# Performance work log

Hardware: AMD Instinct MI355X
Metric: run time of the kernel (lower is better)

## Reference

```python
import jax, jax.numpy as jnp
import numpy as np

N, D = 1024, 128
NEG_INF = -1e30


def setup_inputs() -> dict:
    key = jax.random.key(0)
    ks = jax.random.split(key, 8)
    s = 0.05
    return {
        "X": jax.random.normal(ks[0], (N, D), dtype=jnp.float32),
        "Wq": jax.random.normal(ks[1], (D, D), dtype=jnp.float32) * s,
        "Wk": jax.random.normal(ks[2], (D, D), dtype=jnp.float32) * s,
        "v": jax.random.normal(ks[3], (D,), dtype=jnp.float32) * s,
        "w_ih": jax.random.normal(ks[4], (3 * D, 2 * D), dtype=jnp.float32) * s,
        "w_hh": jax.random.normal(ks[5], (3 * D, D), dtype=jnp.float32) * s,
        "b_ih": jax.random.normal(ks[6], (3 * D,), dtype=jnp.float32) * s,
        "b_hh": jax.random.normal(ks[7], (3 * D,), dtype=jnp.float32) * s,
    }


def reference(X, Wq, Wk, v, w_ih, w_hh, b_ih, b_hh):
    n, d = X.shape
    # --- anti-causal additive attention (query i attends keys j >= i) ---
    q = X @ Wq.T                                   # (N, d)
    k = X @ Wk.T                                   # (N, d)
    # scores[i, j] = v . tanh(q_i + k_j)
    scores = jnp.einsum("ijd,d->ij", jnp.tanh(q[:, None, :] + k[None, :, :]), v)
    mask = jnp.arange(n)[None, :] >= jnp.arange(n)[:, None]   # suffix j >= i
    scores = jnp.where(mask, scores, NEG_INF)
    w = jax.nn.softmax(scores, axis=1)             # (N, N)
    att = w @ X                                    # (N, d) context over keys

    # --- single-layer GRU over the N "time" steps, batch 1 ---
    gru_in = jnp.concatenate((X, att), axis=1)     # (N, 2d)
    gi = gru_in @ w_ih.T + b_ih                    # (N, 3d) input gates, precomputed

    def step(h, gi_t):
        gh = h @ w_hh.T + b_hh                     # (3d,)
        i_r, i_z, i_n = jnp.split(gi_t, 3)
        h_r, h_z, h_n = jnp.split(gh, 3)
        r = jax.nn.sigmoid(i_r + h_r)
        z = jax.nn.sigmoid(i_z + h_z)
        nst = jnp.tanh(i_n + r * h_n)
        h_new = (1.0 - z) * nst + z * h
        return h_new, h_new

    h0 = jnp.zeros((d,), dtype=X.dtype)
    _, out = jax.lax.scan(step, h0, gi)            # (N, d)
    return out
```

## Files before the change

kernel.cpp:

```cpp
#include <hip/hip_runtime.h>
#include <hip/hip_bf16.h>

#define N 1024
#define D 128
#define SB 32
#define NSB (N / SB)

typedef __hip_bfloat16 bf16;
typedef __attribute__((ext_vector_type(8))) short bfx8;
typedef __attribute__((ext_vector_type(4))) float fx4;
typedef __attribute__((ext_vector_type(8))) unsigned short u16x8;

__device__ __forceinline__ float b2f(bf16 x) { return __bfloat162float(x); }
__device__ __forceinline__ short f2bf_bits(float x) {
    bf16 b = __float2bfloat16(x);
    return *reinterpret_cast<short*>(&b);
}
__device__ __forceinline__ float bfbits2f(unsigned short u) {
    return __uint_as_float(((unsigned int)u) << 16);
}
__device__ __forceinline__ float fastrcp(float x) { return __builtin_amdgcn_rcpf(x); }

__device__ __forceinline__ float fast_tanh(float x) {
    float e = __expf(2.f * x);
    return 1.f - 2.f * fastrcp(e + 1.f);
}
__device__ __forceinline__ float fast_sigmoid(float x) {
    return fastrcp(1.f + __expf(-x));
}

__device__ __forceinline__ float sel4(fx4 v, int r) {
    float x = (r & 1) ? v[1] : v[0];
    float y = (r & 1) ? v[3] : v[2];
    return (r & 2) ? y : x;
}

__device__ __forceinline__ void async_copy16(const float* g, void* l) {
    __builtin_amdgcn_global_load_lds((const __attribute__((address_space(1))) void*)g,
                                     (__attribute__((address_space(3))) void*)l, 16, 0, 0);
}

__global__ void sniff_kernel(const unsigned short* __restrict__ xu, int* __restrict__ flag) {
    int l = threadIdx.x;
    int cnt = 0;
#pragma unroll
    for (int k = 0; k < 8; ++k) {
        unsigned short u = xu[2 * (l * 8 + k)];
        int e = (u >> 7) & 0xFF;
        cnt += (e >= 96 && e <= 144) ? 1 : 0;
    }
    for (int off = 32; off > 0; off >>= 1) cnt += __shfl_down(cnt, off);
    if (l == 0) *flag = (cnt > 400) ? 1 : 0;
}

struct ConvArgs {
    const void* p[8];
    float* o[8];
    int n[8];
};
__global__ void convert_kernel(ConvArgs A, const int* __restrict__ flag) {
    int seg = blockIdx.y;
    int n = A.n[seg];
    int isbf = *flag;
    const void* p = A.p[seg];
    float* o = A.o[seg];
    for (int i = blockIdx.x * blockDim.x + threadIdx.x; i < n; i += gridDim.x * blockDim.x) {
        float v = isbf ? b2f(((const bf16*)p)[i]) : ((const float*)p)[i];
        o[i] = v;
    }
}

__global__ void transpose_wih(const float* __restrict__ wih, float* __restrict__ wihT) {
    int id = blockIdx.x * 256 + threadIdx.x;
    int c = id / 384;
    int o = id - c * 384;
    wihT[id] = wih[o * 256 + c];
}

__global__ void qk_kernel(const float* __restrict__ X, const float* __restrict__ Wq,
                          const float* __restrict__ Wk,
                          float* __restrict__ q, float* __restrict__ kT) {
    int i = blockIdx.x & (N - 1);
    bool is_k = blockIdx.x >= N;
    int d = threadIdx.x;
    const float* W = is_k ? Wk : Wq;
    float acc = 0.f;
#pragma unroll 8
    for (int c = 0; c < D; ++c)
        acc += X[i * D + c] * W[d * D + c];
    if (is_k) kT[d * N + i] = acc;
    else      q[i * D + d] = acc;
}

__global__ void __launch_bounds__(256) attn_kernel(const float* __restrict__ q,
                                                   const float* __restrict__ kT,
                                                   const float* __restrict__ v,
                                                   const float* __restrict__ X,
                                                   const float* __restrict__ wihT,
                                                   const float* __restrict__ b_ih,
                                                   float* __restrict__ gi) {
    int i = blockIdx.x;
    __shared__ float qs[D], vs[D], xr[D], al[D];
    __shared__ float wrow[N];
    __shared__ float red[256];
    int t = threadIdx.x;
    if (t < D) { qs[t] = q[i * D + t]; vs[t] = v[t]; xr[t] = X[i * D + t]; }
    __syncthreads();

    float sj[4];
    int cnt = 0;
    float m = -1e30f;
    for (int j = i + t; j < N; j += 256) {
        float s = 0.f;
#pragma unroll 8
        for (int d = 0; d < D; ++d) s += vs[d] * fast_tanh(qs[d] + kT[d * N + j]);
        sj[cnt++] = s;
        m = fmaxf(m, s);
    }
    red[t] = m;
    __syncthreads();
    for (int st = 128; st > 0; st >>= 1) {
        if (t < st) red[t] = fmaxf(red[t], red[t + st]);
        __syncthreads();
    }
    m = red[0];
    __syncthreads();
    float lsum = 0.f;
    {
        int it = 0;
        for (int j = i + t; j < N; j += 256, ++it) {
            float p = __expf(sj[it] - m);
            wrow[j] = p;
            lsum += p;
        }
    }
    red[t] = lsum;
    __syncthreads();
    for (int st = 128; st > 0; st >>= 1) {
        if (t < st) red[t] += red[t + st];
        __syncthreads();
    }
    float inv = fastrcp(red[0]);
    __syncthreads();

    int d = t & 127, half = t >> 7;
    float acc = 0.f;
    for (int j = i + half; j < N; j += 2) acc += wrow[j] * X[j * D + d];
    if (half) red[d] = acc;
    __syncthreads();
    if (!half) al[d] = (acc + red[d]) * inv;
    __syncthreads();

    for (int o = t; o < 3 * D; o += 256) {
        float a2 = b_ih[o];
        const float* wt = wihT + o;
#pragma unroll 8
        for (int c = 0; c < D; ++c) a2 += xr[c] * wt[c * 384];
#pragma unroll 8
        for (int c = 0; c < D; ++c) a2 += al[c] * wt[(D + c) * 384];
        gi[i * 3 * D + o] = a2;
    }
}

__global__ void __launch_bounds__(256, 1) gru_kernel(const float* __restrict__ gi,
                                                     const float* __restrict__ w_hh,
                                                     const float* __restrict__ b_hh,
                                                     void* __restrict__ out,
                                                     const int* __restrict__ flag) {
    __shared__ float gi_lds[2][SB][3 * D];
    __shared__ short hist[SB + 1][D];
    int t = threadIdx.x;
    int w = t >> 6;
    int l = t & 63;
    int q = l >> 4;
    int nn = l & 15;
    int isbf = *flag;

    bfx8 a[3][2][4];
#pragma unroll
    for (int tau = 0; tau < 3; ++tau)
#pragma unroll
        for (int mqi = 0; mqi < 2; ++mqi)
#pragma unroll
            for (int kc = 0; kc < 4; ++kc) {
                int row = 128 * tau + 16 * (2 * w + mqi) + nn;
                int k0 = 32 * kc + 8 * q;
#pragma unroll
                for (int j = 0; j < 8; ++j)
                    a[tau][mqi][kc][j] = f2bf_bits(w_hh[row * D + k0 + j]);
            }
    fx4 bias[3][2];
#pragma unroll
    for (int tau = 0; tau < 3; ++tau)
#pragma unroll
        for (int mqi = 0; mqi < 2; ++mqi)
#pragma unroll
            for (int r = 0; r < 4; ++r)
                bias[tau][mqi][r] = b_hh[128 * tau + 16 * (2 * w + mqi) + 4 * q + r];

    int rsel = l & 3;
    int mqsel = (l >> 3) & 1;
    int drow = 32 * w + 16 * mqsel + 4 * q + rsel;
    float h = 0.f;

    int fr = 1 + (t >> 3);
    int fc = (t & 7) * 16;

    {
        const float* src = gi;
        for (int mm = 0; mm < 12; ++mm) {
            int off = (w * 12 + mm) * 256;
            async_copy16(src + off + (l << 2), (char*)&gi_lds[0][0][0] + off * 4);
        }
    }

    for (int sb = 0; sb < NSB; ++sb) {
        int cb = sb & 1;
        if (sb == 0) {
            if (t < 64) ((int*)&hist[0][0])[t] = 0;
        } else {
            u16x8 h0 = *(const u16x8*)&hist[fr][fc];
            u16x8 h1 = *(const u16x8*)&hist[fr][fc + 8];
            int orow = (sb - 1) * SB + fr - 1;
            if (isbf) {
                *(u16x8*)((unsigned short*)out + orow * D + fc) = h0;
                *(u16x8*)((unsigned short*)out + orow * D + fc + 8) = h1;
            } else {
                float* op = (float*)out + orow * D + fc;
                fx4 f0, f1, f2, f3;
#pragma unroll
                for (int j = 0; j < 4; ++j) {
                    f0[j] = bfbits2f(h0[j]);     f1[j] = bfbits2f(h0[4 + j]);
                    f2[j] = bfbits2f(h1[j]);     f3[j] = bfbits2f(h1[4 + j]);
                }
                *(fx4*)op = f0; *(fx4*)(op + 4) = f1;
                *(fx4*)(op + 8) = f2; *(fx4*)(op + 12) = f3;
            }
            if (t < 64) ((int*)&hist[0][0])[t] = ((const int*)&hist[SB][0])[t];
        }
        asm volatile("s_waitcnt vmcnt(0) lgkmcnt(0)\ns_barrier" ::: "memory");

        if (sb + 1 < NSB) {
            const float* src = gi + (size_t)(sb + 1) * SB * 3 * D;
            for (int mm = 0; mm < 12; ++mm) {
                int off = (w * 12 + mm) * 256;
                async_copy16(src + off + (l << 2), (char*)&gi_lds[cb ^ 1][0][0] + off * 4);
            }
        }

        const char* hrd = (const char*)&hist[0][0] + 16 * q;
        const float* gp = &gi_lds[cb][0][0] + drow;
        short* hwr = &hist[1][0] + drow;

        for (int s = 0; s < SB; ++s) {
            bfx8 b0 = *(const bfx8*)(hrd);
            bfx8 b1 = *(const bfx8*)(hrd + 64);
            bfx8 b2 = *(const bfx8*)(hrd + 128);
            bfx8 b3 = *(const bfx8*)(hrd + 192);
            float gr = gp[0];
            float gz = gp[D];
            float gn = gp[2 * D];

            fx4 acc[3][2];
#pragma unroll
            for (int tau = 0; tau < 3; ++tau)
#pragma unroll
                for (int mqi = 0; mqi < 2; ++mqi) {
                    fx4 c = bias[tau][mqi];
                    c = __builtin_amdgcn_mfma_f32_16x16x32_bf16(a[tau][mqi][0], b0, c, 0, 0, 0);
                    c = __builtin_amdgcn_mfma_f32_16x16x32_bf16(a[tau][mqi][1], b1, c, 0, 0, 0);
                    c = __builtin_amdgcn_mfma_f32_16x16x32_bf16(a[tau][mqi][2], b2, c, 0, 0, 0);
                    c = __builtin_amdgcn_mfma_f32_16x16x32_bf16(a[tau][mqi][3], b3, c, 0, 0, 0);
                    acc[tau][mqi] = c;
                }

            float ar = sel4(mqsel ? acc[0][1] : acc[0][0], rsel);
            float az = sel4(mqsel ? acc[1][1] : acc[1][0], rsel);
            float an = sel4(mqsel ? acc[2][1] : acc[2][0], rsel);
            float rr = fast_sigmoid(gr + ar);
            float zz = fast_sigmoid(gz + az);
            float nst = fast_tanh(gn + rr * an);
            h = (1.f - zz) * nst + zz * h;
            *hwr = f2bf_bits(h);

            hrd += 256;
            gp += 3 * D;
            hwr += D;
            asm volatile("s_waitcnt lgkmcnt(0)\ns_barrier" ::: "memory");
        }
    }
    {
        u16x8 h0 = *(const u16x8*)&hist[fr][fc];
        u16x8 h1 = *(const u16x8*)&hist[fr][fc + 8];
        int orow = (NSB - 1) * SB + fr - 1;
        if (isbf) {
            *(u16x8*)((unsigned short*)out + orow * D + fc) = h0;
            *(u16x8*)((unsigned short*)out + orow * D + fc + 8) = h1;
        } else {
            float* op = (float*)out + orow * D + fc;
            fx4 f0, f1, f2, f3;
#pragma unroll
            for (int j = 0; j < 4; ++j) {
                f0[j] = bfbits2f(h0[j]);     f1[j] = bfbits2f(h0[4 + j]);
                f2[j] = bfbits2f(h1[j]);     f3[j] = bfbits2f(h1[4 + j]);
            }
            *(fx4*)op = f0; *(fx4*)(op + 4) = f1;
            *(fx4*)(op + 8) = f2; *(fx4*)(op + 12) = f3;
        }
    }
}

extern "C" void kernel_launch(void* const* d_in, const int* in_sizes, int n_in,
                              void* d_out, int out_size, void* d_ws, size_t ws_size,
                              hipStream_t stream) {
    (void)in_sizes; (void)n_in; (void)out_size; (void)ws_size;

    float* w0 = (float*)d_ws;
    int*   flag = (int*)w0;
    float* Xf   = w0 + 16;
    float* Wqf  = Xf   + N * D;
    float* Wkf  = Wqf  + D * D;
    float* vf   = Wkf  + D * D;
    float* wihf = vf   + D;
    float* whhf = wihf + 3 * D * 2 * D;
    float* bihf = whhf + 3 * D * D;
    float* bhhf = bihf + 3 * D;
    float* q    = bhhf + 3 * D;
    float* kT   = q    + N * D;
    float* wihT = kT   + N * D;
    float* gi   = wihT + 3 * D * 2 * D;

    sniff_kernel<<<1, 64, 0, stream>>>((const unsigned short*)d_in[0], flag);

    ConvArgs A;
    A.p[0] = d_in[0]; A.o[0] = Xf;   A.n[0] = N * D;
    A.p[1] = d_in[1]; A.o[1] = Wqf;  A.n[1] = D * D;
    A.p[2] = d_in[2]; A.o[2] = Wkf;  A.n[2] = D * D;
    A.p[3] = d_in[3]; A.o[3] = vf;   A.n[3] = D;
    A.p[4] = d_in[4]; A.o[4] = wihf; A.n[4] = 3 * D * 2 * D;
    A.p[5] = d_in[5]; A.o[5] = whhf; A.n[5] = 3 * D * D;
    A.p[6] = d_in[6]; A.o[6] = bihf; A.n[6] = 3 * D;
    A.p[7] = d_in[7]; A.o[7] = bhhf; A.n[7] = 3 * D;
    dim3 cgrid(128, 8, 1);
    convert_kernel<<<cgrid, 256, 0, stream>>>(A, flag);

    transpose_wih<<<(3 * D * 2 * D) / 256, 256, 0, stream>>>(wihf, wihT);
    qk_kernel<<<2 * N, D, 0, stream>>>(Xf, Wqf, Wkf, q, kT);
    attn_kernel<<<N, 256, 0, stream>>>(q, kT, vf, Xf, wihT, bihf, gi);
    gru_kernel<<<1, 256, 0, stream>>>(gi, whhf, bhhf, d_out, flag);
}
```

Measured before the change: 632.2 us.

## Fuse attention and GRU into one kernel with per-superblock atomic flags

Merges the attention/gi kernel and the sequential GRU kernel into a single launch. Block 0 runs the GRU and spins on per-32-row completion counters that the attention blocks raise with release atomics, so the recurrence can start before all of gi is ready. Block 0 is the lowest block index, so it likely gets scheduled early and the serial GRU overlaps the attention work. It also restructures the prefetch and barrier waitcnts and reorders the gate MFMAs so the r gate is ready earlier. The risks are spin-wait overhead and a deadlock if the attention blocks cannot be scheduled while block 0 polls, plus a larger LDS footprint for every attention block.

```diff
diff --git a/kernel.cpp b/kernel.cpp
--- a/kernel.cpp
+++ b/kernel.cpp
@@ -40,17 +40,26 @@
                                      (__attribute__((address_space(3))) void*)l, 16, 0, 0);
 }
 
-__global__ void sniff_kernel(const unsigned short* __restrict__ xu, int* __restrict__ flag) {
+__device__ __forceinline__ void wait_rows(int* cnt, int sb) {
+    while (__hip_atomic_load(&cnt[sb], __ATOMIC_ACQUIRE, __HIP_MEMORY_SCOPE_AGENT) < SB)
+        __builtin_amdgcn_s_sleep(2);
+}
+
+#define MFMA(A, B, C) __builtin_amdgcn_mfma_f32_16x16x32_bf16((A), (B), (C), 0, 0, 0)
+
+__global__ void sniff_kernel(const unsigned short* __restrict__ xu, int* __restrict__ flag,
+                             int* __restrict__ cnt) {
     int l = threadIdx.x;
-    int cnt = 0;
+    if (l < NSB) cnt[l] = 0;
+    int c = 0;
 #pragma unroll
     for (int k = 0; k < 8; ++k) {
         unsigned short u = xu[2 * (l * 8 + k)];
         int e = (u >> 7) & 0xFF;
-        cnt += (e >= 96 && e <= 144) ? 1 : 0;
-    }
-    for (int off = 32; off > 0; off >>= 1) cnt += __shfl_down(cnt, off);
-    if (l == 0) *flag = (cnt > 400) ? 1 : 0;
+        c += (e >= 96 && e <= 144) ? 1 : 0;
+    }
+    for (int off = 32; off > 0; off >>= 1) c += __shfl_down(c, off);
+    if (l == 0) *flag = (c > 400) ? 1 : 0;
 }
 
 struct ConvArgs {
@@ -92,87 +101,95 @@
     else      q[i * D + d] = acc;
 }
 
-__global__ void __launch_bounds__(256) attn_kernel(const float* __restrict__ q,
-                                                   const float* __restrict__ kT,
-                                                   const float* __restrict__ v,
-                                                   const float* __restrict__ X,
-                                                   const float* __restrict__ wihT,
-                                                   const float* __restrict__ b_ih,
-                                                   float* __restrict__ gi) {
-    int i = blockIdx.x;
-    __shared__ float qs[D], vs[D], xr[D], al[D];
-    __shared__ float wrow[N];
-    __shared__ float red[256];
+__global__ void __launch_bounds__(256, 1) fused_kernel(
+        const float* __restrict__ q, const float* __restrict__ kT,
+        const float* __restrict__ v, const float* __restrict__ X,
+        const float* __restrict__ wihT, const float* __restrict__ b_ih,
+        float* __restrict__ gi,
+        const float* __restrict__ w_hh, const float* __restrict__ b_hh,
+        void* __restrict__ out, const int* __restrict__ flag,
+        int* __restrict__ cnt) {
+    __shared__ __align__(16) char smem[2 * SB * 3 * D * 4 + (SB + 1) * D * 2];
     int t = threadIdx.x;
-    if (t < D) { qs[t] = q[i * D + t]; vs[t] = v[t]; xr[t] = X[i * D + t]; }
-    __syncthreads();
-
-    float sj[4];
-    int cnt = 0;
-    float m = -1e30f;
-    for (int j = i + t; j < N; j += 256) {
-        float s = 0.f;
+
+    if (blockIdx.x != 0) {
+        int i = blockIdx.x - 1;
+        float* qs   = (float*)smem;
+        float* vs   = qs + D;
+        float* xr   = vs + D;
+        float* al   = xr + D;
+        float* wrow = al + D;
+        float* red  = wrow + N;
+
+        if (t < D) { qs[t] = q[i * D + t]; vs[t] = v[t]; xr[t] = X[i * D + t]; }
+        __syncthreads();
+
+        float sj[4];
+        int nj = 0;
+        float m = -1e30f;
+        for (int j = i + t; j < N; j += 256) {
+            float s = 0.f;
 #pragma unroll 8
-        for (int d = 0; d < D; ++d) s += vs[d] * fast_tanh(qs[d] + kT[d * N + j]);
-        sj[cnt++] = s;
-        m = fmaxf(m, s);
-    }
-    red[t] = m;
-    __syncthreads();
-    for (int st = 128; st > 0; st >>= 1) {
-        if (t < st) red[t] = fmaxf(red[t], red[t + st]);
-        __syncthreads();
-    }
-    m = red[0];
-    __syncthreads();
-    float lsum = 0.f;
-    {
-        int it = 0;
-        for (int j = i + t; j < N; j += 256, ++it) {
-            float p = __expf(sj[it] - m);
-            wrow[j] = p;
-            lsum += p;
-        }
-    }
-    red[t] = lsum;
-    __syncthreads();
-    for (int st = 128; st > 0; st >>= 1) {
-        if (t < st) red[t] += red[t + st];
-        __syncthreads();
-    }
-    float inv = fastrcp(red[0]);
-    __syncthreads();
-
-    int d = t & 127, half = t >> 7;
-    float acc = 0.f;
-    for (int j = i + half; j < N; j += 2) acc += wrow[j] * X[j * D + d];
-    if (half) red[d] = acc;
-    __syncthreads();
-    if (!half) al[d] = (acc + red[d]) * inv;
-    __syncthreads();
-
-    for (int o = t; o < 3 * D; o += 256) {
-        float a2 = b_ih[o];
-        const float* wt = wihT + o;
+            for (int d = 0; d < D; ++d) s += vs[d] * fast_tanh(qs[d] + kT[d * N + j]);
+            sj[nj++] = s;
+            m = fmaxf(m, s);
+        }
+        red[t] = m;
+        __syncthreads();
+        for (int st = 128; st > 0; st >>= 1) {
+            if (t < st) red[t] = fmaxf(red[t], red[t + st]);
+            __syncthreads();
+        }
+        m = red[0];
+        __syncthreads();
+        float lsum = 0.f;
+        {
+            int it = 0;
+            for (int j = i + t; j < N; j += 256, ++it) {
+                float p = __expf(sj[it] - m);
+                wrow[j] = p;
+                lsum += p;
+            }
+        }
+        red[t] = lsum;
+        __syncthreads();
+        for (int st = 128; st > 0; st >>= 1) {
+            if (t < st) red[t] += red[t + st];
+            __syncthreads();
+        }
+        float inv = fastrcp(red[0]);
+        __syncthreads();
+
+        int d = t & 127, half = t >> 7;
+        float acc = 0.f;
+        for (int j = i + half; j < N; j += 2) acc += wrow[j] * X[j * D + d];
+        if (half) red[d] = acc;
+        __syncthreads();
+        if (!half) al[d] = (acc + red[d]) * inv;
+        __syncthreads();
+
+        for (int o = t; o < 3 * D; o += 256) {
+            float a2 = b_ih[o];
+            const float* wt = wihT + o;
 #pragma unroll 8
-        for (int c = 0; c < D; ++c) a2 += xr[c] * wt[c * 384];
+            for (int c = 0; c < D; ++c) a2 += xr[c] * wt[c * 384];
 #pragma unroll 8
-        for (int c = 0; c < D; ++c) a2 += al[c] * wt[(D + c) * 384];
-        gi[i * 3 * D + o] = a2;
-    }
-}
-
-__global__ void __launch_bounds__(256, 1) gru_kernel(const float* __restrict__ gi,
-                                                     const float* __restrict__ w_hh,
-                                                     const float* __restrict__ b_hh,
-                                                     void* __restrict__ out,
-                                                     const int* __restrict__ flag) {
-    __shared__ float gi_lds[2][SB][3 * D];
-    __shared__ short hist[SB + 1][D];
-    int t = threadIdx.x;
+            for (int c = 0; c < D; ++c) a2 += al[c] * wt[(D + c) * 384];
+            gi[i * 3 * D + o] = a2;
+        }
+        __syncthreads();
+        if (t == 0) {
+            __threadfence();
+            __hip_atomic_fetch_add(&cnt[i >> 5], 1, __ATOMIC_RELEASE, __HIP_MEMORY_SCOPE_AGENT);
+        }
+        return;
+    }
+
+    float* gi_lds = (float*)smem;
+    short* hist   = (short*)(smem + 2 * SB * 3 * D * 4);
     int w = t >> 6;
     int l = t & 63;
-    int q = l >> 4;
+    int qq = l >> 4;
     int nn = l & 15;
     int isbf = *flag;
 
@@ -184,7 +201,7 @@
 #pragma unroll
             for (int kc = 0; kc < 4; ++kc) {
                 int row = 128 * tau + 16 * (2 * w + mqi) + nn;
-                int k0 = 32 * kc + 8 * q;
+                int k0 = 32 * kc + 8 * qq;
 #pragma unroll
                 for (int j = 0; j < 8; ++j)
                     a[tau][mqi][kc][j] = f2bf_bits(w_hh[row * D + k0 + j]);
@@ -196,31 +213,44 @@
         for (int mqi = 0; mqi < 2; ++mqi)
 #pragma unroll
             for (int r = 0; r < 4; ++r)
-                bias[tau][mqi][r] = b_hh[128 * tau + 16 * (2 * w + mqi) + 4 * q + r];
+                bias[tau][mqi][r] = b_hh[128 * tau + 16 * (2 * w + mqi) + 4 * qq + r];
 
     int rsel = l & 3;
     int mqsel = (l >> 3) & 1;
-    int drow = 32 * w + 16 * mqsel + 4 * q + rsel;
+    int drow = 32 * w + 16 * mqsel + 4 * qq + rsel;
     float h = 0.f;
 
     int fr = 1 + (t >> 3);
     int fc = (t & 7) * 16;
 
+    wait_rows(cnt, 0);
     {
         const float* src = gi;
         for (int mm = 0; mm < 12; ++mm) {
             int off = (w * 12 + mm) * 256;
-            async_copy16(src + off + (l << 2), (char*)&gi_lds[0][0][0] + off * 4);
+            async_copy16(src + off + (l << 2), smem + off * 4);
         }
     }
 
     for (int sb = 0; sb < NSB; ++sb) {
         int cb = sb & 1;
-        if (sb == 0) {
-            if (t < 64) ((int*)&hist[0][0])[t] = 0;
-        } else {
-            u16x8 h0 = *(const u16x8*)&hist[fr][fc];
-            u16x8 h1 = *(const u16x8*)&hist[fr][fc + 8];
+        u16x8 h0 = 0, h1 = 0;
+        int hcopy = 0;
+        if (sb > 0) {
+            h0 = *(const u16x8*)(hist + fr * D + fc);
+            h1 = *(const u16x8*)(hist + fr * D + fc + 8);
+            if (t < 64) hcopy = ((const int*)(hist + SB * D))[t];
+        }
+        if (sb + 1 < NSB) {
+            wait_rows(cnt, sb + 1);
+            const float* src = gi + (size_t)(sb + 1) * SB * 3 * D;
+            char* dst = smem + (cb ^ 1) * SB * 3 * D * 4;
+            for (int mm = 0; mm < 12; ++mm) {
+                int off = (w * 12 + mm) * 256;
+                async_copy16(src + off + (l << 2), dst + off * 4);
+            }
+        }
+        if (sb > 0) {
             int orow = (sb - 1) * SB + fr - 1;
             if (isbf) {
                 *(u16x8*)((unsigned short*)out + orow * D + fc) = h0;
@@ -236,21 +266,19 @@
                 *(fx4*)op = f0; *(fx4*)(op + 4) = f1;
                 *(fx4*)(op + 8) = f2; *(fx4*)(op + 12) = f3;
             }
-            if (t < 64) ((int*)&hist[0][0])[t] = ((const int*)&hist[SB][0])[t];
-        }
-        asm volatile("s_waitcnt vmcnt(0) lgkmcnt(0)\ns_barrier" ::: "memory");
-
-        if (sb + 1 < NSB) {
-            const float* src = gi + (size_t)(sb + 1) * SB * 3 * D;
-            for (int mm = 0; mm < 12; ++mm) {
-                int off = (w * 12 + mm) * 256;
-                async_copy16(src + off + (l << 2), (char*)&gi_lds[cb ^ 1][0][0] + off * 4);
-            }
-        }
-
-        const char* hrd = (const char*)&hist[0][0] + 16 * q;
-        const float* gp = &gi_lds[cb][0][0] + drow;
-        short* hwr = &hist[1][0] + drow;
+        }
+        if (t < 64) ((int*)hist)[t] = (sb == 0) ? 0 : hcopy;
+
+        if (sb == 0)
+            asm volatile("s_waitcnt vmcnt(12) lgkmcnt(0)\ns_barrier" ::: "memory");
+        else if (sb + 1 < NSB)
+            asm volatile("s_waitcnt vmcnt(16) lgkmcnt(0)\ns_barrier" ::: "memory");
+        else
+            asm volatile("s_waitcnt vmcnt(4) lgkmcnt(0)\ns_barrier" ::: "memory");
+
+        const char* hrd = (const char*)hist + 16 * qq;
+        const float* gp = gi_lds + cb * SB * 3 * D + drow;
+        short* hwr = hist + D + drow;
 
         for (int s = 0; s < SB; ++s) {
             bfx8 b0 = *(const bfx8*)(hrd);
@@ -261,23 +289,28 @@
             float gz = gp[D];
             float gn = gp[2 * D];
 
-            fx4 acc[3][2];
-#pragma unroll
-            for (int tau = 0; tau < 3; ++tau)
-#pragma unroll
-                for (int mqi = 0; mqi < 2; ++mqi) {
-                    fx4 c = bias[tau][mqi];
-                    c = __builtin_amdgcn_mfma_f32_16x16x32_bf16(a[tau][mqi][0], b0, c, 0, 0, 0);
-                    c = __builtin_amdgcn_mfma_f32_16x16x32_bf16(a[tau][mqi][1], b1, c, 0, 0, 0);
-                    c = __builtin_amdgcn_mfma_f32_16x16x32_bf16(a[tau][mqi][2], b2, c, 0, 0, 0);
-                    c = __builtin_amdgcn_mfma_f32_16x16x32_bf16(a[tau][mqi][3], b3, c, 0, 0, 0);
-                    acc[tau][mqi] = c;
-                }
-
-            float ar = sel4(mqsel ? acc[0][1] : acc[0][0], rsel);
-            float az = sel4(mqsel ? acc[1][1] : acc[1][0], rsel);
-            float an = sel4(mqsel ? acc[2][1] : acc[2][0], rsel);
+            fx4 c00 = bias[0][0], c01 = bias[0][1];
+            c00 = MFMA(a[0][0][0], b0, c00); c00 = MFMA(a[0][0][1], b1, c00);
+            c00 = MFMA(a[0][0][2], b2, c00); c00 = MFMA(a[0][0][3], b3, c00);
+            c01 = MFMA(a[0][1][0], b0, c01); c01 = MFMA(a[0][1][1], b1, c01);
+            c01 = MFMA(a[0][1][2], b2, c01); c01 = MFMA(a[0][1][3], b3, c01);
+            float ar = sel4(mqsel ? c01 : c00, rsel);
             float rr = fast_sigmoid(gr + ar);
+
+            fx4 c20 = bias[2][0], c21 = bias[2][1];
+            c20 = MFMA(a[2][0][0], b0, c20); c20 = MFMA(a[2][0][1], b1, c20);
+            c20 = MFMA(a[2][0][2], b2, c20); c20 = MFMA(a[2][0][3], b3, c20);
+            c21 = MFMA(a[2][1][0], b0, c21); c21 = MFMA(a[2][1][1], b1, c21);
+            c21 = MFMA(a[2][1][2], b2, c21); c21 = MFMA(a[2][1][3], b3, c21);
+            float an = sel4(mqsel ? c21 : c20, rsel);
+
+            fx4 c10 = bias[1][0], c11 = bias[1][1];
+            c10 = MFMA(a[1][0][0], b0, c10); c10 = MFMA(a[1][0][1], b1, c10);
+            c10 = MFMA(a[1][0][2], b2, c10); c10 = MFMA(a[1][0][3], b3, c10);
+            c11 = MFMA(a[1][1][0], b0, c11); c11 = MFMA(a[1][1][1], b1, c11);
+            c11 = MFMA(a[1][1][2], b2, c11); c11 = MFMA(a[1][1][3], b3, c11);
+            float az = sel4(mqsel ? c11 : c10, rsel);
+
             float zz = fast_sigmoid(gz + az);
             float nst = fast_tanh(gn + rr * an);
             h = (1.f - zz) * nst + zz * h;
@@ -290,8 +323,8 @@
         }
     }
     {
-        u16x8 h0 = *(const u16x8*)&hist[fr][fc];
-        u16x8 h1 = *(const u16x8*)&hist[fr][fc + 8];
+        u16x8 h0 = *(const u16x8*)(hist + fr * D + fc);
+        u16x8 h1 = *(const u16x8*)(hist + fr * D + fc + 8);
         int orow = (NSB - 1) * SB + fr - 1;
         if (isbf) {
             *(u16x8*)((unsigned short*)out + orow * D + fc) = h0;
@@ -317,7 +350,8 @@
 
     float* w0 = (float*)d_ws;
     int*   flag = (int*)w0;
-    float* Xf   = w0 + 16;
+    int*   cnt  = (int*)w0 + 16;
+    float* Xf   = w0 + 64;
     float* Wqf  = Xf   + N * D;
     float* Wkf  = Wqf  + D * D;
     float* vf   = Wkf  + D * D;
@@ -330,7 +364,7 @@
     float* wihT = kT   + N * D;
     float* gi   = wihT + 3 * D * 2 * D;
 
-    sniff_kernel<<<1, 64, 0, stream>>>((const unsigned short*)d_in[0], flag);
+    sniff_kernel<<<1, 64, 0, stream>>>((const unsigned short*)d_in[0], flag, cnt);
 
     ConvArgs A;
     A.p[0] = d_in[0]; A.o[0] = Xf;   A.n[0] = N * D;
@@ -346,6 +380,6 @@
 
     transpose_wih<<<(3 * D * 2 * D) / 256, 256, 0, stream>>>(wihf, wihT);
     qk_kernel<<<2 * N, D, 0, stream>>>(Xf, Wqf, Wkf, q, kT);
-    attn_kernel<<<N, 256, 0, stream>>>(q, kT, vf, Xf, wihT, bihf, gi);
-    gru_kernel<<<1, 256, 0, stream>>>(gi, whhf, bhhf, d_out, flag);
-}
+    fused_kernel<<<N + 1, 256, 0, stream>>>(q, kT, vf, Xf, wihT, bihf, gi,
+                                            whhf, bhhf, d_out, flag, cnt);
+}
```

New measurement: 707.7 us. 11.9% more time.
